# Kernel tuning notes

Measured on AMD Instinct MI355X. Metric: run time of the kernel, lower is better.

## Reference

```python
import jax, jax.numpy as jnp
import numpy as np

NUM_TOKENS = 16384
DIM = 4096
N_EXPERTS = 256
ROUTE_SCALE = 1.0


def setup_inputs() -> dict:
    key = jax.random.key(0)
    k_x, k_w = jax.random.split(key)
    x = jax.random.normal(k_x, (NUM_TOKENS, DIM), dtype=jnp.float32)
    # nn.init.normal_(weight, std=0.02)
    weight = 0.02 * jax.random.normal(k_w, (N_EXPERTS, DIM), dtype=jnp.float32)
    return {"x": x, "weight": weight}


def reference(x, weight):
    # Router GEMM: [T, D] @ [D, E] -> [T, E]
    scores = jnp.einsum("td,ed->te", x, weight)
    # Eval-mode token_choice path: softmax in fp32
    probs = jax.nn.softmax(scores.astype(jnp.float32), axis=-1)  # [T, E]
    indices = jnp.argmax(probs, axis=-1, keepdims=True)  # [T, 1] int
    # Hard one-hot scatter of argmax
    y_hard = jax.nn.one_hot(indices[:, 0], N_EXPERTS, dtype=probs.dtype)  # [T, E]
    # Straight-through estimator mix
    ste = jax.lax.stop_gradient(y_hard - probs) + probs
    # Gather routing weight at the selected expert
    weights = jnp.take_along_axis(ste, indices, axis=-1)  # [T, 1]
    weights = (weights * ROUTE_SCALE).astype(x.dtype)
    return weights, indices
```

## Files before the change

kernel.cpp:

```cpp
#include <hip/hip_runtime.h>
#include <stdint.h>

#define NUM_TOKENS 16384
#define DIM        4096
#define NEXP       256
#define MB         32
#define BK         64
#define NITER      (DIM / BK)
#define APAD       72
#define NWAVES     8
#define MARGIN     0.025f
#define CAP        16384

typedef __attribute__((ext_vector_type(4))) float   f32x4;
typedef __attribute__((ext_vector_type(8))) __bf16  bf16x8;

static __device__ __forceinline__ unsigned short f32_to_bf16(float f) {
    unsigned int u = __float_as_uint(f);
    u += 0x7fffu + ((u >> 16) & 1u);
    return (unsigned short)(u >> 16);
}

__global__ void cvt_weights(const float* __restrict__ w,
                            unsigned short* __restrict__ wh,
                            int* __restrict__ counter) {
    if (blockIdx.x == 0 && threadIdx.x == 0) *counter = 0;
    const int n4 = NEXP * DIM / 4;
    const int stride = gridDim.x * blockDim.x;
    for (int i = blockIdx.x * blockDim.x + threadIdx.x; i < n4; i += stride) {
        float4 v = ((const float4*)w)[i];
        ushort4 h;
        h.x = f32_to_bf16(v.x); h.y = f32_to_bf16(v.y);
        h.z = f32_to_bf16(v.z); h.w = f32_to_bf16(v.w);
        ((ushort4*)wh)[i] = h;
    }
}

__global__ __launch_bounds__(512, 4) void gate_main(
    const float* __restrict__ x,
    const unsigned short* __restrict__ wh,
    float* __restrict__ out,
    int* __restrict__ counter,
    int4* __restrict__ entries)
{
    __shared__ unsigned short lAh[2][MB][APAD];
    __shared__ float4 cand[NWAVES][MB];

    const int tid  = threadIdx.x;
    const int wv   = tid >> 6;
    const int lane = tid & 63;
    const int tok0 = blockIdx.x * MB;

    const int ta   = tid >> 4;
    const int kcol = (tid & 15) * 4;
    const float* xrow = x + (size_t)(tok0 + ta) * DIM + kcol;

    const int quad = lane >> 4;
    const int col  = lane & 15;

    const unsigned short* bp[2];
    #pragma unroll
    for (int nt = 0; nt < 2; ++nt)
        bp[nt] = wh + (size_t)(wv * 32 + nt * 16 + col) * DIM + quad * 8;

    f32x4 acc[2][2];
    #pragma unroll
    for (int mt = 0; mt < 2; ++mt)
        #pragma unroll
        for (int nt = 0; nt < 2; ++nt)
            acc[mt][nt] = f32x4{0.f, 0.f, 0.f, 0.f};

    bf16x8 b0[2][2], b1[2][2];
    #pragma unroll
    for (int kk2 = 0; kk2 < 2; ++kk2)
        #pragma unroll
        for (int nt = 0; nt < 2; ++nt)
            b0[kk2][nt] = *(const bf16x8*)(bp[nt] + kk2 * 32);
    #pragma unroll
    for (int kk2 = 0; kk2 < 2; ++kk2)
        #pragma unroll
        for (int nt = 0; nt < 2; ++nt)
            b1[kk2][nt] = *(const bf16x8*)(bp[nt] + BK + kk2 * 32);
    __builtin_amdgcn_sched_barrier(0);
    float4 x0 = *(const float4*)(xrow);
    float4 r0 = *(const float4*)(xrow + 1 * BK);
    float4 r1 = *(const float4*)(xrow + 2 * BK);
    float4 r2 = *(const float4*)(xrow + 3 * BK);
    float4 r3 = *(const float4*)(xrow + 4 * BK);
    {
        ushort4 h;
        h.x = f32_to_bf16(x0.x); h.y = f32_to_bf16(x0.y);
        h.z = f32_to_bf16(x0.z); h.w = f32_to_bf16(x0.w);
        *(ushort4*)&lAh[0][ta][kcol] = h;
    }
    asm volatile("s_waitcnt lgkmcnt(0)" ::: "memory");
    __builtin_amdgcn_s_barrier();
    asm volatile("" ::: "memory");

    auto body = [&](int it, float4& xr, bf16x8 (&bc)[2][2]) {
        const int cur = it & 1;
        const int nxt = cur ^ 1;
        if (it + 1 < NITER) {
            ushort4 h;
            h.x = f32_to_bf16(xr.x); h.y = f32_to_bf16(xr.y);
            h.z = f32_to_bf16(xr.z); h.w = f32_to_bf16(xr.w);
            *(ushort4*)&lAh[nxt][ta][kcol] = h;
        }
        #pragma unroll
        for (int kk2 = 0; kk2 < 2; ++kk2) {
            bf16x8 ah0 = *(const bf16x8*)&lAh[cur][col][kk2 * 32 + quad * 8];
            bf16x8 ah1 = *(const bf16x8*)&lAh[cur][16 + col][kk2 * 32 + quad * 8];
            acc[0][0] = __builtin_amdgcn_mfma_f32_16x16x32_bf16(ah0, bc[kk2][0], acc[0][0], 0, 0, 0);
            acc[1][0] = __builtin_amdgcn_mfma_f32_16x16x32_bf16(ah1, bc[kk2][0], acc[1][0], 0, 0, 0);
            acc[0][1] = __builtin_amdgcn_mfma_f32_16x16x32_bf16(ah0, bc[kk2][1], acc[0][1], 0, 0, 0);
            acc[1][1] = __builtin_amdgcn_mfma_f32_16x16x32_bf16(ah1, bc[kk2][1], acc[1][1], 0, 0, 0);
            if (it + 2 < NITER) {
                #pragma unroll
                for (int nt = 0; nt < 2; ++nt)
                    bc[kk2][nt] = *(const bf16x8*)(bp[nt] + (it + 2) * BK + kk2 * 32);
            }
        }
        __builtin_amdgcn_sched_barrier(0);
        if (it + 5 < NITER)
            xr = *(const float4*)(xrow + (it + 5) * BK);
        asm volatile("s_waitcnt lgkmcnt(0)" ::: "memory");
        __builtin_amdgcn_s_barrier();
        asm volatile("" ::: "memory");
    };

    #pragma unroll 1
    for (int itb = 0; itb < NITER; itb += 4) {
        body(itb + 0, r0, b0);
        body(itb + 1, r1, b1);
        body(itb + 2, r2, b0);
        body(itb + 3, r3, b1);
    }

    #pragma unroll
    for (int mt = 0; mt < 2; ++mt) {
        #pragma unroll
        for (int r = 0; r < 4; ++r) {
            float s0 = acc[mt][0][r]; int e0 = wv * 32 + col;
            float s1 = acc[mt][1][r]; int e1 = e0 + 16;
            float t1s, t2s; int t1e, t2e;
            if (s1 > s0) { t1s = s1; t1e = e1; t2s = s0; t2e = e0; }
            else         { t1s = s0; t1e = e0; t2s = s1; t2e = e1; }
            #pragma unroll
            for (int m = 1; m <= 8; m <<= 1) {
                float o1s = __shfl_xor(t1s, m); int o1e = __shfl_xor(t1e, m);
                float o2s = __shfl_xor(t2s, m); int o2e = __shfl_xor(t2e, m);
                bool o1_top = (o1s > t1s) || (o1s == t1s && o1e < t1e);
                if (o1_top) {
                    bool keep_t1 = (t1s > o2s) || (t1s == o2s && t1e < o2e);
                    t2s = keep_t1 ? t1s : o2s; t2e = keep_t1 ? t1e : o2e;
                    t1s = o1s; t1e = o1e;
                } else {
                    bool o1_2nd = (o1s > t2s) || (o1s == t2s && o1e < t2e);
                    if (o1_2nd) { t2s = o1s; t2e = o1e; }
                }
            }
            if (col == 0) {
                int tok = mt * 16 + quad * 4 + r;
                cand[wv][tok] = make_float4(t1s, __int_as_float(t1e), t2s, __int_as_float(t2e));
            }
        }
    }
    __syncthreads();

    if (tid < MB) {
        float4 c0 = cand[0][tid];
        float t1s = c0.x; int t1e = __float_as_int(c0.y);
        float t2s = c0.z; int t2e = __float_as_int(c0.w);
        #pragma unroll
        for (int wvi = 1; wvi < NWAVES; ++wvi) {
            float4 c = cand[wvi][tid];
            float o1s = c.x; int o1e = __float_as_int(c.y);
            float o2s = c.z; int o2e = __float_as_int(c.w);
            bool o1_top = (o1s > t1s) || (o1s == t1s && o1e < t1e);
            if (o1_top) {
                bool keep_t1 = (t1s > o2s) || (t1s == o2s && t1e < o2e);
                t2s = keep_t1 ? t1s : o2s; t2e = keep_t1 ? t1e : o2e;
                t1s = o1s; t1e = o1e;
            } else {
                bool o1_2nd = (o1s > t2s) || (o1s == t2s && o1e < t2e);
                if (o1_2nd) { t2s = o1s; t2e = o1e; }
            }
        }
        const int gtok = tok0 + tid;
        out[gtok] = 1.0f;
        out[NUM_TOKENS + gtok] = (float)t1e;
        if (t1s - t2s < MARGIN) {
            int slot = atomicAdd(counter, 1);
            if (slot < CAP) entries[slot] = make_int4(gtok, t1e, t2e, 0);
        }
    }
}

__global__ void refine(const float* __restrict__ x,
                       const float* __restrict__ w,
                       const int* __restrict__ counter,
                       const int4* __restrict__ entries,
                       float* __restrict__ out) {
    const int gwave  = (blockIdx.x * blockDim.x + threadIdx.x) >> 6;
    const int lane   = threadIdx.x & 63;
    const int nwaves = (gridDim.x * blockDim.x) >> 6;
    int n = *counter; if (n > CAP) n = CAP;
    for (int i = gwave; i < n; i += nwaves) {
        int4 e = entries[i];
        const float* xr = x + (size_t)e.x * DIM;
        const float* w1 = w + (size_t)e.y * DIM;
        const float* w2 = w + (size_t)e.z * DIM;
        double d1 = 0.0, d2 = 0.0;
        for (int k = lane; k < DIM; k += 64) {
            double xv = (double)xr[k];
            d1 += xv * (double)w1[k];
            d2 += xv * (double)w2[k];
        }
        #pragma unroll
        for (int m = 32; m > 0; m >>= 1) {
            d1 += __shfl_xor(d1, m);
            d2 += __shfl_xor(d2, m);
        }
        if (lane == 0) {
            int best = (d1 > d2) ? e.y : ((d2 > d1) ? e.z : (e.y < e.z ? e.y : e.z));
            out[NUM_TOKENS + e.x] = (float)best;
        }
    }
}

extern "C" void kernel_launch(void* const* d_in, const int* in_sizes, int n_in,
                              void* d_out, int out_size, void* d_ws, size_t ws_size,
                              hipStream_t stream) {
    const float* x = (const float*)d_in[0];
    const float* w = (const float*)d_in[1];
    float* out = (float*)d_out;

    char* ws = (char*)d_ws;
    unsigned short* wh = (unsigned short*)ws;
    int*  counter = (int*)(ws + (2u << 20));
    int4* entries = (int4*)(ws + (2u << 20) + 16);

    cvt_weights<<<256, 256, 0, stream>>>(w, wh, counter);
    gate_main<<<NUM_TOKENS / MB, 512, 0, stream>>>(x, wh, out, counter, entries);
    refine<<<256, 256, 0, stream>>>(x, w, counter, entries, out);
}
```

Measured before the change: 462.2 us.

## Double token tile per block and pre-swizzle bf16 weights into MFMA fragment order

The gate GEMM block grows from 32 to 64 tokens and from 8 to 16 waves, with each wave owning 16 experts over four M-tiles. Each weight fragment is now reused across twice as many tokens, which halves weight reads per block. The weight conversion kernel writes bf16 weights pre-permuted into per-wave, per-iteration, per-lane fragment order, so B loads become contiguous 16-byte accesses per lane. The x prefetch depth drops from five stages to three to save registers at 1024 threads. In exchange, occupancy is coarser and less latency is hidden on the x stream.

```diff
diff --git a/kernel.cpp b/kernel.cpp
--- a/kernel.cpp
+++ b/kernel.cpp
@@ -4,16 +4,17 @@
 #define NUM_TOKENS 16384
 #define DIM        4096
 #define NEXP       256
-#define MB         32
+#define MB         64
 #define BK         64
 #define NITER      (DIM / BK)
 #define APAD       72
-#define NWAVES     8
+#define NWAVES     16
 #define MARGIN     0.025f
 #define CAP        16384
 
-typedef __attribute__((ext_vector_type(4))) float   f32x4;
-typedef __attribute__((ext_vector_type(8))) __bf16  bf16x8;
+typedef __attribute__((ext_vector_type(4))) float          f32x4;
+typedef __attribute__((ext_vector_type(8))) __bf16         bf16x8;
+typedef __attribute__((ext_vector_type(8))) unsigned short ushort8;
 
 static __device__ __forceinline__ unsigned short f32_to_bf16(float f) {
     unsigned int u = __float_as_uint(f);
@@ -25,18 +26,33 @@
                             unsigned short* __restrict__ wh,
                             int* __restrict__ counter) {
     if (blockIdx.x == 0 && threadIdx.x == 0) *counter = 0;
-    const int n4 = NEXP * DIM / 4;
+    const int n8 = NEXP * DIM / 8;
     const int stride = gridDim.x * blockDim.x;
-    for (int i = blockIdx.x * blockDim.x + threadIdx.x; i < n4; i += stride) {
-        float4 v = ((const float4*)w)[i];
-        ushort4 h;
-        h.x = f32_to_bf16(v.x); h.y = f32_to_bf16(v.y);
-        h.z = f32_to_bf16(v.z); h.w = f32_to_bf16(v.w);
-        ((ushort4*)wh)[i] = h;
-    }
-}
-
-__global__ __launch_bounds__(512, 4) void gate_main(
+    for (int i = blockIdx.x * blockDim.x + threadIdx.x; i < n8; i += stride) {
+        const int e  = i >> 9;
+        const int k8 = i & 511;
+        const int k  = k8 * 8;
+        const int g    = e >> 4;
+        const int col  = e & 15;
+        const int it   = k8 >> 3;
+        const int kk2  = (k8 >> 2) & 1;
+        const int quad = k8 & 3;
+        const int lane = quad * 16 + col;
+        const int s    = ((g * 64 + it) * 2 + kk2) * 64 + lane;
+
+        const float* src = w + (size_t)e * DIM + k;
+        float4 v0 = *(const float4*)(src);
+        float4 v1 = *(const float4*)(src + 4);
+        ushort8 h;
+        h[0] = f32_to_bf16(v0.x); h[1] = f32_to_bf16(v0.y);
+        h[2] = f32_to_bf16(v0.z); h[3] = f32_to_bf16(v0.w);
+        h[4] = f32_to_bf16(v1.x); h[5] = f32_to_bf16(v1.y);
+        h[6] = f32_to_bf16(v1.z); h[7] = f32_to_bf16(v1.w);
+        *(ushort8*)(wh + (size_t)s * 8) = h;
+    }
+}
+
+__global__ __launch_bounds__(1024, 4) void gate_main(
     const float* __restrict__ x,
     const unsigned short* __restrict__ wh,
     float* __restrict__ out,
@@ -58,35 +74,25 @@
     const int quad = lane >> 4;
     const int col  = lane & 15;
 
-    const unsigned short* bp[2];
+    f32x4 acc[4];
     #pragma unroll
-    for (int nt = 0; nt < 2; ++nt)
-        bp[nt] = wh + (size_t)(wv * 32 + nt * 16 + col) * DIM + quad * 8;
-
-    f32x4 acc[2][2];
-    #pragma unroll
-    for (int mt = 0; mt < 2; ++mt)
-        #pragma unroll
-        for (int nt = 0; nt < 2; ++nt)
-            acc[mt][nt] = f32x4{0.f, 0.f, 0.f, 0.f};
-
-    bf16x8 b0[2][2], b1[2][2];
-    #pragma unroll
-    for (int kk2 = 0; kk2 < 2; ++kk2)
-        #pragma unroll
-        for (int nt = 0; nt < 2; ++nt)
-            b0[kk2][nt] = *(const bf16x8*)(bp[nt] + kk2 * 32);
-    #pragma unroll
-    for (int kk2 = 0; kk2 < 2; ++kk2)
-        #pragma unroll
-        for (int nt = 0; nt < 2; ++nt)
-            b1[kk2][nt] = *(const bf16x8*)(bp[nt] + BK + kk2 * 32);
+    for (int mt = 0; mt < 4; ++mt)
+        acc[mt] = f32x4{0.f, 0.f, 0.f, 0.f};
+
+    auto ldb = [&](int it, bf16x8 (&bc)[2]) {
+        #pragma unroll
+        for (int kk2 = 0; kk2 < 2; ++kk2)
+            bc[kk2] = *(const bf16x8*)(wh +
+                ((((size_t)wv * 64 + it) * 2 + kk2) * 64 + lane) * 8);
+    };
+
+    bf16x8 bA[2], bB[2];
+    ldb(0, bA);
+    ldb(1, bB);
     __builtin_amdgcn_sched_barrier(0);
-    float4 x0 = *(const float4*)(xrow);
-    float4 r0 = *(const float4*)(xrow + 1 * BK);
-    float4 r1 = *(const float4*)(xrow + 2 * BK);
-    float4 r2 = *(const float4*)(xrow + 3 * BK);
-    float4 r3 = *(const float4*)(xrow + 4 * BK);
+    float4 x0  = *(const float4*)(xrow);
+    float4 xva = *(const float4*)(xrow + 1 * BK);
+    float4 xvb = *(const float4*)(xrow + 2 * BK);
     {
         ushort4 h;
         h.x = f32_to_bf16(x0.x); h.y = f32_to_bf16(x0.y);
@@ -97,7 +103,7 @@
     __builtin_amdgcn_s_barrier();
     asm volatile("" ::: "memory");
 
-    auto body = [&](int it, float4& xr, bf16x8 (&bc)[2][2]) {
+    auto body = [&](int it, float4& xr, bf16x8 (&bc)[2]) {
         const int cur = it & 1;
         const int nxt = cur ^ 1;
         if (it + 1 < NITER) {
@@ -108,43 +114,37 @@
         }
         #pragma unroll
         for (int kk2 = 0; kk2 < 2; ++kk2) {
-            bf16x8 ah0 = *(const bf16x8*)&lAh[cur][col][kk2 * 32 + quad * 8];
-            bf16x8 ah1 = *(const bf16x8*)&lAh[cur][16 + col][kk2 * 32 + quad * 8];
-            acc[0][0] = __builtin_amdgcn_mfma_f32_16x16x32_bf16(ah0, bc[kk2][0], acc[0][0], 0, 0, 0);
-            acc[1][0] = __builtin_amdgcn_mfma_f32_16x16x32_bf16(ah1, bc[kk2][0], acc[1][0], 0, 0, 0);
-            acc[0][1] = __builtin_amdgcn_mfma_f32_16x16x32_bf16(ah0, bc[kk2][1], acc[0][1], 0, 0, 0);
-            acc[1][1] = __builtin_amdgcn_mfma_f32_16x16x32_bf16(ah1, bc[kk2][1], acc[1][1], 0, 0, 0);
-            if (it + 2 < NITER) {
-                #pragma unroll
-                for (int nt = 0; nt < 2; ++nt)
-                    bc[kk2][nt] = *(const bf16x8*)(bp[nt] + (it + 2) * BK + kk2 * 32);
-            }
-        }
+            bf16x8 ah[4];
+            #pragma unroll
+            for (int mt = 0; mt < 4; ++mt)
+                ah[mt] = *(const bf16x8*)&lAh[cur][mt * 16 + col][kk2 * 32 + quad * 8];
+            #pragma unroll
+            for (int mt = 0; mt < 4; ++mt)
+                acc[mt] = __builtin_amdgcn_mfma_f32_16x16x32_bf16(
+                    ah[mt], bc[kk2], acc[mt], 0, 0, 0);
+        }
+        if (it + 2 < NITER)
+            ldb(it + 2, bc);
         __builtin_amdgcn_sched_barrier(0);
-        if (it + 5 < NITER)
-            xr = *(const float4*)(xrow + (it + 5) * BK);
+        if (it + 3 < NITER)
+            xr = *(const float4*)(xrow + (it + 3) * BK);
         asm volatile("s_waitcnt lgkmcnt(0)" ::: "memory");
         __builtin_amdgcn_s_barrier();
         asm volatile("" ::: "memory");
     };
 
     #pragma unroll 1
-    for (int itb = 0; itb < NITER; itb += 4) {
-        body(itb + 0, r0, b0);
-        body(itb + 1, r1, b1);
-        body(itb + 2, r2, b0);
-        body(itb + 3, r3, b1);
+    for (int itb = 0; itb < NITER; itb += 2) {
+        body(itb + 0, xva, bA);
+        body(itb + 1, xvb, bB);
     }
 
     #pragma unroll
-    for (int mt = 0; mt < 2; ++mt) {
+    for (int mt = 0; mt < 4; ++mt) {
         #pragma unroll
         for (int r = 0; r < 4; ++r) {
-            float s0 = acc[mt][0][r]; int e0 = wv * 32 + col;
-            float s1 = acc[mt][1][r]; int e1 = e0 + 16;
-            float t1s, t2s; int t1e, t2e;
-            if (s1 > s0) { t1s = s1; t1e = e1; t2s = s0; t2e = e0; }
-            else         { t1s = s0; t1e = e0; t2s = s1; t2e = e1; }
+            float t1s = acc[mt][r]; int t1e = wv * 16 + col;
+            float t2s = -__builtin_inff(); int t2e = 0x7fffffff;
             #pragma unroll
             for (int m = 1; m <= 8; m <<= 1) {
                 float o1s = __shfl_xor(t1s, m); int o1e = __shfl_xor(t1e, m);
@@ -241,6 +241,6 @@
     int4* entries = (int4*)(ws + (2u << 20) + 16);
 
     cvt_weights<<<256, 256, 0, stream>>>(w, wh, counter);
-    gate_main<<<NUM_TOKENS / MB, 512, 0, stream>>>(x, wh, out, counter, entries);
+    gate_main<<<NUM_TOKENS / MB, 1024, 0, stream>>>(x, wh, out, counter, entries);
     refine<<<256, 256, 0, stream>>>(x, w, counter, entries, out);
 }
```

New measurement: 435.5 us. 1.06x faster.
